# Kernel tuning notes

Hardware: AMD Instinct MI355X
Metric: run time of the kernel (lower is better)

Reference implementation:

```python
import jax, jax.numpy as jnp
import numpy as np


def setup_inputs() -> dict:
    key = jax.random.key(0)
    k1, k2 = jax.random.split(key)
    B, T, D = 16, 512, 384
    x = jax.random.normal(k1, (B, T, D), dtype=jnp.float32)
    durations = jax.random.randint(k2, (B, T), 0, 8, dtype=jnp.int64)
    return {"x": x, "durations": durations, "max_len": 4096}


def reference(x, durations, max_len):
    # x: [B, T, D], durations: [B, T] int, max_len: static int
    # Each phoneme t is repeated durations[b, t] times along the frame axis,
    # then sequences are zero-padded to a common length.
    cum = jnp.cumsum(durations, axis=1)              # [B, T] exclusive upper bounds
    frames = jnp.arange(max_len)                     # [F]
    # frame f belongs to phoneme idx where cum[idx-1] <= f < cum[idx]
    idx = jax.vmap(lambda c: jnp.searchsorted(c, frames, side="right"))(cum)  # [B, F]
    valid = frames[None, :] < cum[:, -1][:, None]    # [B, F] frames past total -> pad
    idx = jnp.minimum(idx, durations.shape[1] - 1)   # clamp out-of-range gather
    out = jnp.take_along_axis(x, idx[:, :, None], axis=1)  # [B, F, D]
    return jnp.where(valid[:, :, None], out, jnp.zeros((), dtype=x.dtype))
```

## Files before the change

kernel.cpp:

```cpp
#include <hip/hip_runtime.h>

#define BB    16
#define TT    512
#define FF    4096
#define DD4   96
#define NTHR  256
#define FPB   64
#define CHUNKS (FF / FPB)
#define NBLK  (BB * CHUNKS)
#define NXCD  8

typedef float f4 __attribute__((ext_vector_type(4)));

__global__ __launch_bounds__(NTHR) void lenreg_kernel(
    const f4* __restrict__ x, const int* __restrict__ dur,
    f4* __restrict__ out) {

    int bid = blockIdx.x;
    bid = (bid & (NXCD - 1)) * (NBLK / NXCD) + (bid >> 3);

    const int b     = bid >> 6;
    const int chunk = bid & (CHUNKS - 1);
    const int t     = threadIdx.x;
    const int lane  = t & 63;
    const int wid   = t >> 6;

    __shared__ int s_cum[TT];
    __shared__ int s_ws[NTHR / 64];

    const int2 dd = ((const int2*)(dur + b * TT))[t];
    int v = dd.x + dd.y;
#pragma unroll
    for (int off = 1; off < 64; off <<= 1) {
        int u = __shfl_up(v, off, 64);
        if (lane >= off) v += u;
    }
    if (lane == 63) s_ws[wid] = v;
    __syncthreads();
    int base = 0;
#pragma unroll
    for (int w = 0; w < NTHR / 64 - 1; ++w)
        if (w < wid) base += s_ws[w];
    const int c1 = base + v;
    s_cum[2 * t]     = c1 - dd.y;
    s_cum[2 * t + 1] = c1;
    __syncthreads();

    const int total = s_cum[TT - 1];
    const int fl    = t >> 4;
    const int c0    = t & 15;
    const int fbase = chunk * FPB;

    int idx0, idx1, idx2, idx3;
    {
        int ii[4];
#pragma unroll
        for (int it = 0; it < 4; ++it) {
            const int f = fbase + it * 16 + fl;
            int idx = 0;
#pragma unroll
            for (int step = 256; step > 0; step >>= 1) {
                if (idx + step <= TT && s_cum[idx + step - 1] <= f) idx += step;
            }
            ii[it] = idx;
        }
        idx0 = ii[0]; idx1 = ii[1]; idx2 = ii[2]; idx3 = ii[3];
    }

#pragma unroll
    for (int it = 0; it < 4; ++it) {
        const int idx = (it == 0) ? idx0 : (it == 1) ? idx1 : (it == 2) ? idx2 : idx3;
        const int f   = fbase + it * 16 + fl;
        f4* dst = out + ((size_t)b * FF + f) * DD4;
        if (f < total) {
            const f4* src = x + ((size_t)b * TT + idx) * DD4;
#pragma unroll
            for (int k = 0; k < 6; ++k)
                __builtin_nontemporal_store(src[c0 + 16 * k], &dst[c0 + 16 * k]);
        } else {
            const f4 z = {0.f, 0.f, 0.f, 0.f};
#pragma unroll
            for (int k = 0; k < 6; ++k)
                __builtin_nontemporal_store(z, &dst[c0 + 16 * k]);
        }
    }
}

extern "C" void kernel_launch(void* const* d_in, const int* in_sizes, int n_in,
                              void* d_out, int out_size, void* d_ws, size_t ws_size,
                              hipStream_t stream) {
    const float* x = (const float*)d_in[0];
    const int* dur = (const int*)d_in[1];
    (void)d_ws; (void)ws_size;

    lenreg_kernel<<<NBLK, NTHR, 0, stream>>>(
        (const f4*)x, dur, (f4*)d_out);
}
```

Before: 126.3 us.

## Compute frame indices once into shared memory and use flat coalesced copy

After: 125.3 us (median of 2 runs). Within noise of the previous version (-0.8%).

```diff
diff --git a/kernel.cpp b/kernel.cpp
--- a/kernel.cpp
+++ b/kernel.cpp
@@ -8,6 +8,7 @@
 #define FPB   64
 #define CHUNKS (FF / FPB)
 #define NBLK  (BB * CHUNKS)
+#define PPB   (FPB * DD4)
 #define NXCD  8
 
 typedef float f4 __attribute__((ext_vector_type(4)));
@@ -27,6 +28,7 @@
 
     __shared__ int s_cum[TT];
     __shared__ int s_ws[NTHR / 64];
+    __shared__ int s_idx[FPB];
 
     const int2 dd = ((const int2*)(dur + b * TT))[t];
     int v = dd.x + dd.y;
@@ -47,42 +49,28 @@
     __syncthreads();
 
     const int total = s_cum[TT - 1];
-    const int fl    = t >> 4;
-    const int c0    = t & 15;
     const int fbase = chunk * FPB;
 
-    int idx0, idx1, idx2, idx3;
-    {
-        int ii[4];
+    if (t < FPB) {
+        const int f = fbase + t;
+        int idx = 0;
 #pragma unroll
-        for (int it = 0; it < 4; ++it) {
-            const int f = fbase + it * 16 + fl;
-            int idx = 0;
+        for (int step = 256; step > 0; step >>= 1)
+            if (idx + step <= TT && s_cum[idx + step - 1] <= f) idx += step;
+        s_idx[t] = idx < TT - 1 ? idx : TT - 1;
+    }
+    __syncthreads();
+
+    const f4* xb = x + (size_t)b * TT * DD4;
+    f4* ob = out + (size_t)(b * FF + fbase) * DD4;
 #pragma unroll
-            for (int step = 256; step > 0; step >>= 1) {
-                if (idx + step <= TT && s_cum[idx + step - 1] <= f) idx += step;
-            }
-            ii[it] = idx;
-        }
-        idx0 = ii[0]; idx1 = ii[1]; idx2 = ii[2]; idx3 = ii[3];
-    }
-
-#pragma unroll
-    for (int it = 0; it < 4; ++it) {
-        const int idx = (it == 0) ? idx0 : (it == 1) ? idx1 : (it == 2) ? idx2 : idx3;
-        const int f   = fbase + it * 16 + fl;
-        f4* dst = out + ((size_t)b * FF + f) * DD4;
-        if (f < total) {
-            const f4* src = x + ((size_t)b * TT + idx) * DD4;
-#pragma unroll
-            for (int k = 0; k < 6; ++k)
-                __builtin_nontemporal_store(src[c0 + 16 * k], &dst[c0 + 16 * k]);
-        } else {
-            const f4 z = {0.f, 0.f, 0.f, 0.f};
-#pragma unroll
-            for (int k = 0; k < 6; ++k)
-                __builtin_nontemporal_store(z, &dst[c0 + 16 * k]);
-        }
+    for (int k = 0; k < PPB / NTHR; ++k) {
+        const int p = t + NTHR * k;
+        const int f = p / DD4;
+        const int c = p - f * DD4;
+        f4 val = {0.f, 0.f, 0.f, 0.f};
+        if (fbase + f < total) val = xb[s_idx[f] * DD4 + c];
+        ob[p] = val;
     }
 }
 
```
